# Performance work log

Measured on AMD Instinct MI355X. Metric: run time of the kernel, lower is better.

Reference implementation:

```python
import jax, jax.numpy as jnp
import numpy as np

# Qwen3MoeSparseMLPBlock config
T = 2048            # tokens
H = 2048            # hidden_size
I = 768             # moe_intermediate_size
E = 32              # num_experts
K = 8               # num_experts_per_tok
CAP = 1024          # per-expert capacity = 2 * (T*K/E); routing is ~uniform so never overflows


def setup_inputs() -> dict:
    key = jax.random.key(0)
    k1, k2, k3, k4, k5 = jax.random.split(key, 5)
    hidden_states = jax.random.normal(k1, (T, H), dtype=jnp.float32)
    gate_w = jax.random.normal(k2, (H, E), dtype=jnp.float32) / np.sqrt(H)
    gate_b = 0.01 * jax.random.normal(k3, (E,), dtype=jnp.float32)
    w_gate_up = jax.random.normal(k4, (E, H, 2 * I), dtype=jnp.float32) / np.sqrt(H)
    w_down = jax.random.normal(k5, (E, I, H), dtype=jnp.float32) / np.sqrt(I)
    return {"hidden_states": hidden_states, "gate_w": gate_w, "gate_b": gate_b,
            "w_gate_up": w_gate_up, "w_down": w_down}


def _moe(x, gate_w, gate_b, w_gate_up, w_down):
    # router: softmax in fp32, top-k, renormalize (norm_topk_prob=True)
    logits = x @ gate_w + gate_b                                   # [T, E]
    probs = jax.nn.softmax(logits.astype(jnp.float32), axis=-1)
    vals, idx = jax.lax.top_k(probs, K)                            # [T, K]
    vals = vals / jnp.sum(vals, axis=-1, keepdims=True)

    # token permutation: sort the T*K (token, expert) assignments by expert id
    A = T * K
    e_flat = idx.reshape(-1)                                       # [A] expert id per assignment
    t_flat = jnp.arange(A, dtype=jnp.int32) // K                   # [A] token id per assignment
    order = jnp.argsort(e_flat)                                    # assignments grouped by expert
    counts = jnp.bincount(e_flat, length=E)                        # [E] tokens per expert
    starts = jnp.cumsum(counts) - counts                           # [E] group offsets

    # fixed-capacity windows into the sorted assignment list (rows beyond count masked)
    win = jnp.minimum(starts[:, None] + jnp.arange(CAP)[None, :], A - 1)   # [E, CAP]
    valid = (jnp.arange(CAP)[None, :] < counts[:, None]).astype(x.dtype)   # [E, CAP]
    tok = t_flat[order][win]                                       # [E, CAP] source token ids
    w = vals.reshape(-1)[order][win] * valid                       # [E, CAP] routing weights (0 on pads)

    # gather -> grouped FFN (SiluAndMul) -> weighted scatter-add combine
    xb = x[tok]                                                    # [E, CAP, H]
    gu = jnp.einsum('ech,ehf->ecf', xb, w_gate_up)                 # [E, CAP, 2I]
    g, u = jnp.split(gu, 2, axis=-1)
    h = jax.nn.silu(g) * u                                         # [E, CAP, I]
    yb = jnp.einsum('eci,eih->ech', h, w_down) * w[..., None]      # [E, CAP, H]
    out = jnp.zeros_like(x).at[tok.reshape(-1)].add(yb.reshape(-1, H))
    return out


def reference(hidden_states, gate_w, gate_b, w_gate_up, w_down):
    return _moe(hidden_states, gate_w, gate_b, w_gate_up, w_down)
```

## Files before the change

kernel.cpp:

```cpp
#include <hip/hip_runtime.h>
#include <math.h>

#define TT 2048
#define HH 2048
#define ID 768
#define NE 32
#define KTOP 8
#define CAP 1024

typedef short bf16x8 __attribute__((ext_vector_type(8)));
typedef float f32x4 __attribute__((ext_vector_type(4)));

__device__ __forceinline__ unsigned short f2b(float f) {
  unsigned int u = __builtin_bit_cast(unsigned int, f);
  u += 0x7fff + ((u >> 16) & 1);
  return (unsigned short)(u >> 16);
}

__device__ __forceinline__ void gload16(const unsigned short* g, void* l) {
  __builtin_amdgcn_global_load_lds(
      (const __attribute__((address_space(1))) unsigned int*)g,
      (__attribute__((address_space(3))) unsigned int*)l, 16, 0, 0);
}

__global__ __launch_bounds__(256) void cvt_x_kernel(const float* __restrict__ x,
                                                    unsigned short* __restrict__ xb) {
  const size_t i = ((size_t)blockIdx.x * 256 + threadIdx.x) * 8;
  const float4 a = *(const float4*)(x + i);
  const float4 b = *(const float4*)(x + i + 4);
  union { unsigned short us[8]; uint4 v; } p;
  p.us[0] = f2b(a.x); p.us[1] = f2b(a.y); p.us[2] = f2b(a.z); p.us[3] = f2b(a.w);
  p.us[4] = f2b(b.x); p.us[5] = f2b(b.y); p.us[6] = f2b(b.z); p.us[7] = f2b(b.w);
  *(uint4*)(xb + i) = p.v;
}

__global__ __launch_bounds__(256) void cvt_w_kernel(const float* __restrict__ in,
                                                    unsigned short* __restrict__ out,
                                                    int R, int C) {
  __shared__ float tile[64][65];
  const int e = blockIdx.z;
  const int r0 = blockIdx.y * 64, c0 = blockIdx.x * 64;
  const int tid = threadIdx.x;
  const float* src = in + (size_t)e * R * C;
  const int rr = tid >> 4, c4 = tid & 15;
#pragma unroll
  for (int it = 0; it < 4; ++it) {
    const int r = it * 16 + rr;
    const float4 v = *(const float4*)(src + (size_t)(r0 + r) * C + c0 + c4 * 4);
    tile[r][c4 * 4 + 0] = v.x; tile[r][c4 * 4 + 1] = v.y;
    tile[r][c4 * 4 + 2] = v.z; tile[r][c4 * 4 + 3] = v.w;
  }
  __syncthreads();
  unsigned short* dst = out + (size_t)e * R * C;
#pragma unroll
  for (int it = 0; it < 2; ++it) {
    const int task = tid + it * 256;
    const int c = task >> 3, g = task & 7;
    union { unsigned short us[8]; uint4 v; } p;
#pragma unroll
    for (int j = 0; j < 8; ++j) p.us[j] = f2b(tile[g * 8 + j][c]);
    *(uint4*)(dst + (size_t)(c0 + c) * R + r0 + g * 8) = p.v;
  }
}

__global__ __launch_bounds__(256) void router_kernel(
    const float* __restrict__ x, const float* __restrict__ gw,
    const float* __restrict__ gb, int* __restrict__ counts,
    int* __restrict__ tok_slot, float* __restrict__ w_slot) {
  const int t = blockIdx.x;
  const int tid = threadIdx.x;
  const int e = tid & 31;
  const int c = tid >> 5;
  const float* xr = x + (size_t)t * HH;

  __shared__ double pl[8][NE];
  __shared__ float logits[NE];

  double a0 = 0.0, a1 = 0.0, a2 = 0.0, a3 = 0.0;
  const int j0 = c * 256;
#pragma unroll 4
  for (int j = 0; j < 256; j += 4) {
    const int jj = j0 + j;
    a0 = fma((double)xr[jj + 0], (double)gw[(size_t)(jj + 0) * NE + e], a0);
    a1 = fma((double)xr[jj + 1], (double)gw[(size_t)(jj + 1) * NE + e], a1);
    a2 = fma((double)xr[jj + 2], (double)gw[(size_t)(jj + 2) * NE + e], a2);
    a3 = fma((double)xr[jj + 3], (double)gw[(size_t)(jj + 3) * NE + e], a3);
  }
  pl[c][e] = (a0 + a1) + (a2 + a3);
  __syncthreads();

  if (tid < NE) {
    double s = 0.0;
    for (int cc = 0; cc < 8; ++cc) s += pl[cc][tid];
    logits[tid] = (float)s + gb[tid];
  }
  __syncthreads();

  if (tid == 0) {
    float l[NE];
    float m = -1e30f;
    for (int i = 0; i < NE; ++i) { l[i] = logits[i]; m = fmaxf(m, l[i]); }
    int sel[KTOP]; float ex[KTOP]; float s = 0.f;
    for (int k = 0; k < KTOP; ++k) {
      float best = -1e30f; int bi = 0;
      for (int i = 0; i < NE; ++i)
        if (l[i] > best) { best = l[i]; bi = i; }
      sel[k] = bi;
      ex[k] = expf(best - m);
      s += ex[k];
      l[bi] = -1e31f;
    }
    const float inv = 1.f / s;
    for (int k = 0; k < KTOP; ++k) {
      const int ee = sel[k];
      const int pos = atomicAdd(&counts[ee], 1);
      if (pos < CAP) {
        tok_slot[ee * CAP + pos] = t;
        w_slot[ee * CAP + pos] = ex[k] * inv;
      }
    }
  }
}


__global__ __launch_bounds__(256) void gu2_kernel(
    const unsigned short* __restrict__ xb, const unsigned short* __restrict__ wguT,
    const int* __restrict__ counts, const int* __restrict__ tok_slot,
    unsigned short* __restrict__ h_ws) {
  const int e = blockIdx.z, mt = blockIdx.y, nt = blockIdx.x;
  int cnt = counts[e]; cnt = cnt > CAP ? CAP : cnt;
  if (mt * 128 >= cnt) return;

  __shared__ __align__(16) unsigned short As[128 * 32];
  __shared__ __align__(16) unsigned short Bg[64 * 32];
  __shared__ __align__(16) unsigned short Bu[64 * 32];
  __shared__ int toks[128];

  const int tid = threadIdx.x;
  if (tid < 128) toks[tid] = tok_slot[e * CAP + mt * 128 + tid];
  __syncthreads();

  const unsigned short* bgp = wguT + (size_t)e * (2 * ID) * HH + (size_t)(nt * 64) * HH;
  const unsigned short* bup = bgp + (size_t)ID * HH;

  const int wv = tid >> 6;
  const int ar = tid >> 2, cg = tid & 3;
  char* ldsA0 = (char*)As + wv * 1024;
  char* ldsA1 = (char*)As + 4096 + wv * 1024;
  char* ldsBg = (char*)Bg + wv * 1024;
  char* ldsBu = (char*)Bu + wv * 1024;
  const unsigned short* srcA0 = xb + (size_t)toks[ar] * HH + cg * 8;
  const unsigned short* srcA1 = xb + (size_t)toks[ar + 64] * HH + cg * 8;
  const unsigned short* srcBg = bgp + (size_t)ar * HH + cg * 8;
  const unsigned short* srcBu = bup + (size_t)ar * HH + cg * 8;

  const int wid = tid >> 6, lane = tid & 63;
  const int wm = wid & 1, wn = wid >> 1;
  const int lr = lane & 15, quad = lane >> 4;

  f32x4 accg[4][2], accu[4][2];
  for (int s = 0; s < 4; ++s)
    for (int t = 0; t < 2; ++t)
      for (int r = 0; r < 4; ++r) { accg[s][t][r] = 0.f; accu[s][t][r] = 0.f; }

  for (int k0 = 0; k0 < HH; k0 += 32) {
    gload16(srcA0 + k0, ldsA0);
    gload16(srcA1 + k0, ldsA1);
    gload16(srcBg + k0, ldsBg);
    gload16(srcBu + k0, ldsBu);
    __syncthreads();
    bf16x8 af[4];
#pragma unroll
    for (int s = 0; s < 4; ++s)
      af[s] = *(const bf16x8*)&As[(wm * 64 + s * 16 + lr) * 32 + quad * 8];
#pragma unroll
    for (int t = 0; t < 2; ++t) {
      const bf16x8 bg = *(const bf16x8*)&Bg[(wn * 32 + t * 16 + lr) * 32 + quad * 8];
      const bf16x8 bu = *(const bf16x8*)&Bu[(wn * 32 + t * 16 + lr) * 32 + quad * 8];
#pragma unroll
      for (int s = 0; s < 4; ++s) {
        accg[s][t] = __builtin_amdgcn_mfma_f32_16x16x32_bf16(af[s], bg, accg[s][t], 0, 0, 0);
        accu[s][t] = __builtin_amdgcn_mfma_f32_16x16x32_bf16(af[s], bu, accu[s][t], 0, 0, 0);
      }
    }
    __syncthreads();
  }

  unsigned short* hb = h_ws + (size_t)(e * CAP + mt * 128) * ID + nt * 64;
#pragma unroll
  for (int s = 0; s < 4; ++s)
#pragma unroll
    for (int t = 0; t < 2; ++t)
#pragma unroll
      for (int r = 0; r < 4; ++r) {
        const int row = wm * 64 + s * 16 + quad * 4 + r;
        const int col = wn * 32 + t * 16 + lr;
        const float g = accg[s][t][r], u = accu[s][t][r];
        const float h = (g / (1.f + __expf(-g))) * u;
        hb[(size_t)row * ID + col] = f2b(h);
      }
}

__global__ __launch_bounds__(256) void down2_kernel(
    const unsigned short* __restrict__ h_ws, const unsigned short* __restrict__ wdT,
    const int* __restrict__ counts, const int* __restrict__ tok_slot,
    const float* __restrict__ w_slot, float* __restrict__ out) {
  const int e = blockIdx.z, mt = blockIdx.y;
  const int nb = blockIdx.x * 128;
  int cnt = counts[e]; cnt = cnt > CAP ? CAP : cnt;
  if (mt * 128 >= cnt) return;

  __shared__ __align__(16) unsigned short As[128 * 32];
  __shared__ __align__(16) unsigned short Bs[128 * 32];
  __shared__ int toks[128];
  __shared__ float wr[128];

  const int tid = threadIdx.x;
  if (tid < 128) {
    toks[tid] = tok_slot[e * CAP + mt * 128 + tid];
    wr[tid] = w_slot[e * CAP + mt * 128 + tid];
  }
  __syncthreads();

  const unsigned short* hb = h_ws + (size_t)(e * CAP + mt * 128) * ID;
  const unsigned short* wb = wdT + (size_t)e * HH * ID + (size_t)nb * ID;

  const int wv = tid >> 6;
  const int ar = tid >> 2, cg = tid & 3;
  char* ldsA0 = (char*)As + wv * 1024;
  char* ldsA1 = (char*)As + 4096 + wv * 1024;
  char* ldsB0 = (char*)Bs + wv * 1024;
  char* ldsB1 = (char*)Bs + 4096 + wv * 1024;
  const unsigned short* srcA0 = hb + (size_t)ar * ID + cg * 8;
  const unsigned short* srcA1 = hb + (size_t)(ar + 64) * ID + cg * 8;
  const unsigned short* srcB0 = wb + (size_t)ar * ID + cg * 8;
  const unsigned short* srcB1 = wb + (size_t)(ar + 64) * ID + cg * 8;

  const int wid = tid >> 6, lane = tid & 63;
  const int wm = wid & 1, wn = wid >> 1;
  const int lr = lane & 15, quad = lane >> 4;

  f32x4 acc[4][4];
  for (int s = 0; s < 4; ++s)
    for (int t = 0; t < 4; ++t)
      for (int r = 0; r < 4; ++r) acc[s][t][r] = 0.f;

  for (int k0 = 0; k0 < ID; k0 += 32) {
    gload16(srcA0 + k0, ldsA0);
    gload16(srcA1 + k0, ldsA1);
    gload16(srcB0 + k0, ldsB0);
    gload16(srcB1 + k0, ldsB1);
    __syncthreads();
    bf16x8 af[4], bfr[4];
#pragma unroll
    for (int s = 0; s < 4; ++s)
      af[s] = *(const bf16x8*)&As[(wm * 64 + s * 16 + lr) * 32 + quad * 8];
#pragma unroll
    for (int t = 0; t < 4; ++t)
      bfr[t] = *(const bf16x8*)&Bs[(wn * 64 + t * 16 + lr) * 32 + quad * 8];
#pragma unroll
    for (int s = 0; s < 4; ++s)
#pragma unroll
      for (int t = 0; t < 4; ++t)
        acc[s][t] = __builtin_amdgcn_mfma_f32_16x16x32_bf16(af[s], bfr[t], acc[s][t], 0, 0, 0);
    __syncthreads();
  }

#pragma unroll
  for (int s = 0; s < 4; ++s) {
#pragma unroll
    for (int r = 0; r < 4; ++r) {
      const int row = wm * 64 + s * 16 + quad * 4 + r;
      const float w = wr[row];
      if (w != 0.f) {
        const int tk = toks[row];
        float* op = out + (size_t)tk * HH + nb + wn * 64 + lr;
#pragma unroll
        for (int t = 0; t < 4; ++t)
          atomicAdd(op + t * 16, acc[s][t][r] * w);
      }
    }
  }
}


__global__ __launch_bounds__(256) void gu_kernel(
    const unsigned short* __restrict__ xb, const float* __restrict__ wgu,
    const int* __restrict__ counts, const int* __restrict__ tok_slot,
    unsigned short* __restrict__ h_ws) {
  const int e = blockIdx.z, mt = blockIdx.y, nt = blockIdx.x;
  int cnt = counts[e]; cnt = cnt > CAP ? CAP : cnt;
  if (mt * 128 >= cnt) return;

  __shared__ __align__(16) unsigned short As[128][40];
  __shared__ __align__(16) unsigned short Bg[64][40];
  __shared__ __align__(16) unsigned short Bu[64][40];
  __shared__ int toks[128];

  const int tid = threadIdx.x;
  if (tid < 128) toks[tid] = tok_slot[e * CAP + mt * 128 + tid];
  __syncthreads();

  const float* wg = wgu + (size_t)e * HH * (2 * ID) + nt * 64;
  const float* wu = wg + ID;

  const int wid = tid >> 6, lane = tid & 63;
  const int wm = wid & 1, wn = wid >> 1;
  const int lr = lane & 15, quad = lane >> 4;

  f32x4 accg[4][2], accu[4][2];
  for (int s = 0; s < 4; ++s)
    for (int t = 0; t < 2; ++t)
      for (int r = 0; r < 4; ++r) { accg[s][t][r] = 0.f; accu[s][t][r] = 0.f; }

  for (int k0 = 0; k0 < HH; k0 += 32) {
#pragma unroll
    for (int it = 0; it < 2; ++it) {
      const int task = tid + it * 256;
      const int row = task >> 2, cg = task & 3;
      const uint4 v = *(const uint4*)(xb + (size_t)toks[row] * HH + k0 + cg * 8);
      *(uint4*)&As[row][cg * 8] = v;
    }
#pragma unroll
    for (int it = 0; it < 2; ++it) {
      const int task = tid + it * 256;
      const int k = task >> 4, cg = task & 15;
      const size_t off = (size_t)(k0 + k) * (2 * ID) + cg * 4;
      const float4 vg = *(const float4*)(wg + off);
      const float4 vu = *(const float4*)(wu + off);
      Bg[cg * 4 + 0][k] = f2b(vg.x); Bg[cg * 4 + 1][k] = f2b(vg.y);
      Bg[cg * 4 + 2][k] = f2b(vg.z); Bg[cg * 4 + 3][k] = f2b(vg.w);
      Bu[cg * 4 + 0][k] = f2b(vu.x); Bu[cg * 4 + 1][k] = f2b(vu.y);
      Bu[cg * 4 + 2][k] = f2b(vu.z); Bu[cg * 4 + 3][k] = f2b(vu.w);
    }
    __syncthreads();
    bf16x8 af[4];
#pragma unroll
    for (int s = 0; s < 4; ++s)
      af[s] = *(const bf16x8*)&As[wm * 64 + s * 16 + lr][quad * 8];
#pragma unroll
    for (int t = 0; t < 2; ++t) {
      const bf16x8 bg = *(const bf16x8*)&Bg[wn * 32 + t * 16 + lr][quad * 8];
      const bf16x8 bu = *(const bf16x8*)&Bu[wn * 32 + t * 16 + lr][quad * 8];
#pragma unroll
      for (int s = 0; s < 4; ++s) {
        accg[s][t] = __builtin_amdgcn_mfma_f32_16x16x32_bf16(af[s], bg, accg[s][t], 0, 0, 0);
        accu[s][t] = __builtin_amdgcn_mfma_f32_16x16x32_bf16(af[s], bu, accu[s][t], 0, 0, 0);
      }
    }
    __syncthreads();
  }

  unsigned short* hb = h_ws + (size_t)(e * CAP + mt * 128) * ID + nt * 64;
#pragma unroll
  for (int s = 0; s < 4; ++s)
#pragma unroll
    for (int t = 0; t < 2; ++t)
#pragma unroll
      for (int r = 0; r < 4; ++r) {
        const int row = wm * 64 + s * 16 + quad * 4 + r;
        const int col = wn * 32 + t * 16 + lr;
        const float g = accg[s][t][r], u = accu[s][t][r];
        const float h = (g / (1.f + __expf(-g))) * u;
        hb[(size_t)row * ID + col] = f2b(h);
      }
}

__global__ __launch_bounds__(256) void down_kernel(
    const unsigned short* __restrict__ h_ws, const float* __restrict__ wd,
    const int* __restrict__ counts, const int* __restrict__ tok_slot,
    const float* __restrict__ w_slot, float* __restrict__ out) {
  const int e = blockIdx.z, mt = blockIdx.y;
  const int nb = blockIdx.x * 128;
  int cnt = counts[e]; cnt = cnt > CAP ? CAP : cnt;
  if (mt * 128 >= cnt) return;

  __shared__ __align__(16) unsigned short As[128][40];
  __shared__ __align__(16) unsigned short Bs[128][40];
  __shared__ int toks[128];
  __shared__ float wr[128];

  const int tid = threadIdx.x;
  if (tid < 128) {
    toks[tid] = tok_slot[e * CAP + mt * 128 + tid];
    wr[tid] = w_slot[e * CAP + mt * 128 + tid];
  }

  const unsigned short* hb = h_ws + (size_t)(e * CAP + mt * 128) * ID;
  const float* wb = wd + (size_t)e * ID * HH + nb;

  const int wid = tid >> 6, lane = tid & 63;
  const int wm = wid & 1, wn = wid >> 1;
  const int lr = lane & 15, quad = lane >> 4;

  f32x4 acc[4][4];
  for (int s = 0; s < 4; ++s)
    for (int t = 0; t < 4; ++t)
      for (int r = 0; r < 4; ++r) acc[s][t][r] = 0.f;

  for (int k0 = 0; k0 < ID; k0 += 32) {
#pragma unroll
    for (int it = 0; it < 2; ++it) {
      const int task = tid + it * 256;
      const int row = task >> 2, cg = task & 3;
      const uint4 v = *(const uint4*)(hb + (size_t)row * ID + k0 + cg * 8);
      *(uint4*)&As[row][cg * 8] = v;
    }
#pragma unroll
    for (int it = 0; it < 4; ++it) {
      const int task = tid + it * 256;
      const int k = task >> 5, cg = task & 31;
      const float4 v = *(const float4*)(wb + (size_t)(k0 + k) * HH + cg * 4);
      Bs[cg * 4 + 0][k] = f2b(v.x); Bs[cg * 4 + 1][k] = f2b(v.y);
      Bs[cg * 4 + 2][k] = f2b(v.z); Bs[cg * 4 + 3][k] = f2b(v.w);
    }
    __syncthreads();
    bf16x8 af[4], bfr[4];
#pragma unroll
    for (int s = 0; s < 4; ++s)
      af[s] = *(const bf16x8*)&As[wm * 64 + s * 16 + lr][quad * 8];
#pragma unroll
    for (int t = 0; t < 4; ++t)
      bfr[t] = *(const bf16x8*)&Bs[wn * 64 + t * 16 + lr][quad * 8];
#pragma unroll
    for (int s = 0; s < 4; ++s)
#pragma unroll
      for (int t = 0; t < 4; ++t)
        acc[s][t] = __builtin_amdgcn_mfma_f32_16x16x32_bf16(af[s], bfr[t], acc[s][t], 0, 0, 0);
    __syncthreads();
  }

#pragma unroll
  for (int s = 0; s < 4; ++s) {
#pragma unroll
    for (int r = 0; r < 4; ++r) {
      const int row = wm * 64 + s * 16 + quad * 4 + r;
      const float w = wr[row];
      if (w != 0.f) {
        const int tk = toks[row];
        float* op = out + (size_t)tk * HH + nb + wn * 64 + lr;
#pragma unroll
        for (int t = 0; t < 4; ++t)
          atomicAdd(op + t * 16, acc[s][t][r] * w);
      }
    }
  }
}

extern "C" void kernel_launch(void* const* d_in, const int* in_sizes, int n_in,
                              void* d_out, int out_size, void* d_ws, size_t ws_size,
                              hipStream_t stream) {
  const float* x   = (const float*)d_in[0];
  const float* gw  = (const float*)d_in[1];
  const float* gb  = (const float*)d_in[2];
  const float* wgu = (const float*)d_in[3];
  const float* wd  = (const float*)d_in[4];
  float* out = (float*)d_out;

  char* ws = (char*)d_ws;
  int*   counts   = (int*)ws;
  int*   tok_slot = (int*)(ws + 256);
  float* w_slot   = (float*)(ws + 256 + 131072);
  unsigned short* xb   = (unsigned short*)(ws + 262656);
  unsigned short* h_ws = (unsigned short*)(ws + 8651264);
  unsigned short* wguT = (unsigned short*)(ws + 58982912);
  unsigned short* wdT  = (unsigned short*)(ws + 260309504);
  const size_t NEED = 360972800ULL;

  hipMemsetAsync(d_ws, 0, 262400, stream);
  hipMemsetAsync(d_out, 0, (size_t)out_size * sizeof(float), stream);

  cvt_x_kernel<<<dim3((TT * HH) / (256 * 8)), dim3(256), 0, stream>>>(x, xb);
  router_kernel<<<dim3(TT), dim3(256), 0, stream>>>(x, gw, gb, counts, tok_slot, w_slot);

  if (ws_size >= NEED) {
    cvt_w_kernel<<<dim3((2 * ID) / 64, HH / 64, NE), dim3(256), 0, stream>>>(wgu, wguT, HH, 2 * ID);
    cvt_w_kernel<<<dim3(HH / 64, ID / 64, NE), dim3(256), 0, stream>>>(wd, wdT, ID, HH);
    gu2_kernel<<<dim3(ID / 64, CAP / 128, NE), dim3(256), 0, stream>>>(xb, wguT, counts, tok_slot, h_ws);
    down2_kernel<<<dim3(HH / 128, CAP / 128, NE), dim3(256), 0, stream>>>(h_ws, wdT, counts, tok_slot, w_slot, out);
  } else {
    gu_kernel<<<dim3(ID / 64, CAP / 128, NE), dim3(256), 0, stream>>>(xb, wgu, counts, tok_slot, h_ws);
    down_kernel<<<dim3(HH / 128, CAP / 128, NE), dim3(256), 0, stream>>>(h_ws, wd, counts, tok_slot, w_slot, out);
  }
}
```

Baseline: 1.147 ms.

## Replace grouped GEMMs with 256x256 double-buffered, swizzled, 8-wave MFMA kernels

Rewrites the gate-up and down grouped GEMM kernels to use 512-thread blocks computing 256x256 output tiles with 64-wide K steps. Global-to-LDS loads are double-buffered and interleaved with MFMA quadrants under manual barriers and vmcnt waits, and the LDS layout uses an XOR swizzle to avoid bank conflicts. The gate-up weights are reordered during conversion so gate and up columns sit in interleaved 128-column blocks, letting one tile produce both halves for SiLU fusion. The bigger tiles add data reuse and hide load latency, at the cost of high LDS and register pressure and wasted work on partially filled 256-row tiles.

```diff
diff --git a/kernel.cpp b/kernel.cpp
--- a/kernel.cpp
+++ b/kernel.cpp
@@ -22,6 +22,9 @@
       (const __attribute__((address_space(1))) unsigned int*)g,
       (__attribute__((address_space(3))) unsigned int*)l, 16, 0, 0);
 }
+
+#define SBAR() asm volatile("s_barrier" ::: "memory")
+#define VMCNT(n) asm volatile("s_waitcnt vmcnt(" #n ")" ::: "memory")
 
 __global__ __launch_bounds__(256) void cvt_x_kernel(const float* __restrict__ x,
                                                     unsigned short* __restrict__ xb) {
@@ -60,6 +63,37 @@
 #pragma unroll
     for (int j = 0; j < 8; ++j) p.us[j] = f2b(tile[g * 8 + j][c]);
     *(uint4*)(dst + (size_t)(c0 + c) * R + r0 + g * 8) = p.v;
+  }
+}
+
+__global__ __launch_bounds__(256) void cvt_wgu_kernel(const float* __restrict__ in,
+                                                      unsigned short* __restrict__ out) {
+  __shared__ float tile[64][65];
+  const int e = blockIdx.z;
+  const int r0 = blockIdx.y * 64, c0 = blockIdx.x * 64;
+  const int tid = threadIdx.x;
+  const float* src = in + (size_t)e * HH * (2 * ID);
+  const int rr = tid >> 4, c4 = tid & 15;
+#pragma unroll
+  for (int it = 0; it < 4; ++it) {
+    const int r = it * 16 + rr;
+    const float4 v = *(const float4*)(src + (size_t)(r0 + r) * (2 * ID) + c0 + c4 * 4);
+    tile[r][c4 * 4 + 0] = v.x; tile[r][c4 * 4 + 1] = v.y;
+    tile[r][c4 * 4 + 2] = v.z; tile[r][c4 * 4 + 3] = v.w;
+  }
+  __syncthreads();
+  unsigned short* dst = out + (size_t)e * HH * (2 * ID);
+#pragma unroll
+  for (int it = 0; it < 2; ++it) {
+    const int task = tid + it * 256;
+    const int c = task >> 3, g = task & 7;
+    const int n = c0 + c;
+    const int dr = (n < ID) ? ((n >> 7) * 256 + (n & 127))
+                            : (((n - ID) >> 7) * 256 + 128 + ((n - ID) & 127));
+    union { unsigned short us[8]; uint4 v; } p;
+#pragma unroll
+    for (int j = 0; j < 8; ++j) p.us[j] = f2b(tile[g * 8 + j][c]);
+    *(uint4*)(dst + (size_t)dr * HH + r0 + g * 8) = p.v;
   }
 }
 
@@ -123,164 +157,262 @@
 }
 
 
-__global__ __launch_bounds__(256) void gu2_kernel(
+#define STG_A(nb, half, k0)                                                   \
+  do {                                                                        \
+    gload16(A_src[(half) * 2 + 0] + (k0), &Asb[nb][half][w * 512]);           \
+    gload16(A_src[(half) * 2 + 1] + (k0), &Asb[nb][half][4096 + w * 512]);    \
+  } while (0)
+#define STG_B(nb, half, k0)                                                   \
+  do {                                                                        \
+    gload16(B_src[(half) * 2 + 0] + (k0), &Bsb[nb][half][w * 512]);           \
+    gload16(B_src[(half) * 2 + 1] + (k0), &Bsb[nb][half][4096 + w * 512]);    \
+  } while (0)
+
+#define MFMA16(QM, QN)                                                        \
+  do {                                                                        \
+    _Pragma("unroll")                                                         \
+    for (int m = 0; m < 4; ++m) {                                             \
+      _Pragma("unroll")                                                       \
+      for (int n = 0; n < 2; ++n) {                                           \
+        acc[QM][QN][m][n] = __builtin_amdgcn_mfma_f32_16x16x32_bf16(          \
+            af[m][0], bf[n][0], acc[QM][QN][m][n], 0, 0, 0);                  \
+        acc[QM][QN][m][n] = __builtin_amdgcn_mfma_f32_16x16x32_bf16(          \
+            af[m][1], bf[n][1], acc[QM][QN][m][n], 0, 0, 0);                  \
+      }                                                                       \
+    }                                                                         \
+  } while (0)
+
+#define LDA(half)                                                             \
+  do {                                                                        \
+    _Pragma("unroll")                                                         \
+    for (int m = 0; m < 4; ++m) {                                             \
+      af[m][0] = *(const bf16x8*)&Asb[buf][half][(arow + m * 16) * 64 + cs0f];\
+      af[m][1] = *(const bf16x8*)&Asb[buf][half][(arow + m * 16) * 64 + cs1f];\
+    }                                                                         \
+  } while (0)
+#define LDB(half)                                                             \
+  do {                                                                        \
+    _Pragma("unroll")                                                         \
+    for (int n = 0; n < 2; ++n) {                                             \
+      bf[n][0] = *(const bf16x8*)&Bsb[buf][half][(brow + n * 16) * 64 + cs0f];\
+      bf[n][1] = *(const bf16x8*)&Bsb[buf][half][(brow + n * 16) * 64 + cs1f];\
+    }                                                                         \
+  } while (0)
+
+__global__ __launch_bounds__(512, 2) void gu3_kernel(
     const unsigned short* __restrict__ xb, const unsigned short* __restrict__ wguT,
     const int* __restrict__ counts, const int* __restrict__ tok_slot,
     unsigned short* __restrict__ h_ws) {
   const int e = blockIdx.z, mt = blockIdx.y, nt = blockIdx.x;
   int cnt = counts[e]; cnt = cnt > CAP ? CAP : cnt;
-  if (mt * 128 >= cnt) return;
-
-  __shared__ __align__(16) unsigned short As[128 * 32];
-  __shared__ __align__(16) unsigned short Bg[64 * 32];
-  __shared__ __align__(16) unsigned short Bu[64 * 32];
-  __shared__ int toks[128];
+  if (mt * 256 >= cnt) return;
+
+  __shared__ __align__(16) unsigned short Asb[2][2][128 * 64];
+  __shared__ __align__(16) unsigned short Bsb[2][2][128 * 64];
 
   const int tid = threadIdx.x;
-  if (tid < 128) toks[tid] = tok_slot[e * CAP + mt * 128 + tid];
-  __syncthreads();
-
-  const unsigned short* bgp = wguT + (size_t)e * (2 * ID) * HH + (size_t)(nt * 64) * HH;
-  const unsigned short* bup = bgp + (size_t)ID * HH;
-
-  const int wv = tid >> 6;
-  const int ar = tid >> 2, cg = tid & 3;
-  char* ldsA0 = (char*)As + wv * 1024;
-  char* ldsA1 = (char*)As + 4096 + wv * 1024;
-  char* ldsBg = (char*)Bg + wv * 1024;
-  char* ldsBu = (char*)Bu + wv * 1024;
-  const unsigned short* srcA0 = xb + (size_t)toks[ar] * HH + cg * 8;
-  const unsigned short* srcA1 = xb + (size_t)toks[ar + 64] * HH + cg * 8;
-  const unsigned short* srcBg = bgp + (size_t)ar * HH + cg * 8;
-  const unsigned short* srcBu = bup + (size_t)ar * HH + cg * 8;
-
-  const int wid = tid >> 6, lane = tid & 63;
-  const int wm = wid & 1, wn = wid >> 1;
+  const int w = tid >> 6, lane = tid & 63;
+  const int wr = w & 1, wc = w >> 1;
   const int lr = lane & 15, quad = lane >> 4;
 
-  f32x4 accg[4][2], accu[4][2];
-  for (int s = 0; s < 4; ++s)
-    for (int t = 0; t < 2; ++t)
-      for (int r = 0; r < 4; ++r) { accg[s][t][r] = 0.f; accu[s][t][r] = 0.f; }
-
-  for (int k0 = 0; k0 < HH; k0 += 32) {
-    gload16(srcA0 + k0, ldsA0);
-    gload16(srcA1 + k0, ldsA1);
-    gload16(srcBg + k0, ldsBg);
-    gload16(srcBu + k0, ldsBu);
-    __syncthreads();
-    bf16x8 af[4];
-#pragma unroll
-    for (int s = 0; s < 4; ++s)
-      af[s] = *(const bf16x8*)&As[(wm * 64 + s * 16 + lr) * 32 + quad * 8];
-#pragma unroll
-    for (int t = 0; t < 2; ++t) {
-      const bf16x8 bg = *(const bf16x8*)&Bg[(wn * 32 + t * 16 + lr) * 32 + quad * 8];
-      const bf16x8 bu = *(const bf16x8*)&Bu[(wn * 32 + t * 16 + lr) * 32 + quad * 8];
-#pragma unroll
-      for (int s = 0; s < 4; ++s) {
-        accg[s][t] = __builtin_amdgcn_mfma_f32_16x16x32_bf16(af[s], bg, accg[s][t], 0, 0, 0);
-        accu[s][t] = __builtin_amdgcn_mfma_f32_16x16x32_bf16(af[s], bu, accu[s][t], 0, 0, 0);
+  const int ra = tid >> 3, ca = tid & 7;
+  const int cs = (ca ^ (ra & 7)) * 8;
+
+  const int* tsl = tok_slot + e * CAP + mt * 256;
+  const unsigned short* A_src[4];
+  A_src[0] = xb + (size_t)tsl[ra] * HH + cs;
+  A_src[1] = xb + (size_t)tsl[64 + ra] * HH + cs;
+  A_src[2] = xb + (size_t)tsl[128 + ra] * HH + cs;
+  A_src[3] = xb + (size_t)tsl[192 + ra] * HH + cs;
+  const unsigned short* bb = wguT + (size_t)e * (2 * ID) * HH + (size_t)(nt * 256) * HH;
+  const unsigned short* B_src[4];
+  B_src[0] = bb + (size_t)ra * HH + cs;
+  B_src[1] = bb + (size_t)(64 + ra) * HH + cs;
+  B_src[2] = bb + (size_t)(128 + ra) * HH + cs;
+  B_src[3] = bb + (size_t)(192 + ra) * HH + cs;
+
+  const int cs0f = (quad ^ (lr & 7)) * 8;
+  const int cs1f = ((4 + quad) ^ (lr & 7)) * 8;
+  const int arow = wr * 64 + lr;
+  const int brow = wc * 32 + lr;
+
+  f32x4 acc[2][2][4][2];
+#pragma unroll
+  for (int a = 0; a < 2; ++a)
+#pragma unroll
+    for (int b = 0; b < 2; ++b)
+#pragma unroll
+      for (int m = 0; m < 4; ++m)
+#pragma unroll
+        for (int n = 0; n < 2; ++n)
+#pragma unroll
+          for (int r = 0; r < 4; ++r) acc[a][b][m][n][r] = 0.f;
+
+  STG_A(0, 0, 0); STG_B(0, 0, 0); STG_A(0, 1, 0); STG_B(0, 1, 0);
+  VMCNT(0);
+  SBAR();
+
+  bf16x8 af[4][2], bf[2][2];
+  for (int t = 0; t < 32; ++t) {
+    const int buf = t & 1, nb = buf ^ 1;
+    const int kn = (t + 1) * 64;
+    const bool pf = (t + 1) < 32;
+    LDA(0); LDB(0);
+    if (pf) { STG_A(nb, 0, kn); STG_B(nb, 0, kn); }
+    SBAR();
+    __builtin_amdgcn_s_setprio(1);
+    MFMA16(0, 0);
+    __builtin_amdgcn_s_setprio(0);
+    VMCNT(4);
+    SBAR();
+    LDB(1);
+    if (pf) { STG_A(nb, 1, kn); STG_B(nb, 1, kn); }
+    SBAR();
+    __builtin_amdgcn_s_setprio(1);
+    MFMA16(0, 1);
+    __builtin_amdgcn_s_setprio(0);
+    SBAR();
+    LDA(1); LDB(0);
+    SBAR();
+    __builtin_amdgcn_s_setprio(1);
+    MFMA16(1, 0);
+    __builtin_amdgcn_s_setprio(0);
+    SBAR();
+    LDB(1);
+    SBAR();
+    __builtin_amdgcn_s_setprio(1);
+    MFMA16(1, 1);
+    __builtin_amdgcn_s_setprio(0);
+    VMCNT(2);
+    SBAR();
+  }
+
+  unsigned short* hb = h_ws + ((size_t)e * CAP + mt * 256) * ID + nt * 128;
+#pragma unroll
+  for (int qm = 0; qm < 2; ++qm)
+#pragma unroll
+    for (int m = 0; m < 4; ++m)
+#pragma unroll
+      for (int r = 0; r < 4; ++r) {
+        const int row = qm * 128 + wr * 64 + m * 16 + quad * 4 + r;
+#pragma unroll
+        for (int n = 0; n < 2; ++n) {
+          const float g = acc[qm][0][m][n][r], u = acc[qm][1][m][n][r];
+          const float h = (g / (1.f + __expf(-g))) * u;
+          hb[(size_t)row * ID + wc * 32 + n * 16 + lr] = f2b(h);
+        }
       }
-    }
-    __syncthreads();
-  }
-
-  unsigned short* hb = h_ws + (size_t)(e * CAP + mt * 128) * ID + nt * 64;
-#pragma unroll
-  for (int s = 0; s < 4; ++s)
-#pragma unroll
-    for (int t = 0; t < 2; ++t)
-#pragma unroll
-      for (int r = 0; r < 4; ++r) {
-        const int row = wm * 64 + s * 16 + quad * 4 + r;
-        const int col = wn * 32 + t * 16 + lr;
-        const float g = accg[s][t][r], u = accu[s][t][r];
-        const float h = (g / (1.f + __expf(-g))) * u;
-        hb[(size_t)row * ID + col] = f2b(h);
-      }
-}
-
-__global__ __launch_bounds__(256) void down2_kernel(
+}
+
+__global__ __launch_bounds__(512, 2) void down3_kernel(
     const unsigned short* __restrict__ h_ws, const unsigned short* __restrict__ wdT,
     const int* __restrict__ counts, const int* __restrict__ tok_slot,
     const float* __restrict__ w_slot, float* __restrict__ out) {
-  const int e = blockIdx.z, mt = blockIdx.y;
-  const int nb = blockIdx.x * 128;
+  const int e = blockIdx.z, mt = blockIdx.y, nt = blockIdx.x;
   int cnt = counts[e]; cnt = cnt > CAP ? CAP : cnt;
-  if (mt * 128 >= cnt) return;
-
-  __shared__ __align__(16) unsigned short As[128 * 32];
-  __shared__ __align__(16) unsigned short Bs[128 * 32];
-  __shared__ int toks[128];
-  __shared__ float wr[128];
+  if (mt * 256 >= cnt) return;
+
+  __shared__ __align__(16) unsigned short Asb[2][2][128 * 64];
+  __shared__ __align__(16) unsigned short Bsb[2][2][128 * 64];
 
   const int tid = threadIdx.x;
-  if (tid < 128) {
-    toks[tid] = tok_slot[e * CAP + mt * 128 + tid];
-    wr[tid] = w_slot[e * CAP + mt * 128 + tid];
-  }
-  __syncthreads();
-
-  const unsigned short* hb = h_ws + (size_t)(e * CAP + mt * 128) * ID;
-  const unsigned short* wb = wdT + (size_t)e * HH * ID + (size_t)nb * ID;
-
-  const int wv = tid >> 6;
-  const int ar = tid >> 2, cg = tid & 3;
-  char* ldsA0 = (char*)As + wv * 1024;
-  char* ldsA1 = (char*)As + 4096 + wv * 1024;
-  char* ldsB0 = (char*)Bs + wv * 1024;
-  char* ldsB1 = (char*)Bs + 4096 + wv * 1024;
-  const unsigned short* srcA0 = hb + (size_t)ar * ID + cg * 8;
-  const unsigned short* srcA1 = hb + (size_t)(ar + 64) * ID + cg * 8;
-  const unsigned short* srcB0 = wb + (size_t)ar * ID + cg * 8;
-  const unsigned short* srcB1 = wb + (size_t)(ar + 64) * ID + cg * 8;
-
-  const int wid = tid >> 6, lane = tid & 63;
-  const int wm = wid & 1, wn = wid >> 1;
+  const int w = tid >> 6, lane = tid & 63;
+  const int wr = w & 1, wc = w >> 1;
   const int lr = lane & 15, quad = lane >> 4;
 
-  f32x4 acc[4][4];
-  for (int s = 0; s < 4; ++s)
-    for (int t = 0; t < 4; ++t)
-      for (int r = 0; r < 4; ++r) acc[s][t][r] = 0.f;
-
-  for (int k0 = 0; k0 < ID; k0 += 32) {
-    gload16(srcA0 + k0, ldsA0);
-    gload16(srcA1 + k0, ldsA1);
-    gload16(srcB0 + k0, ldsB0);
-    gload16(srcB1 + k0, ldsB1);
-    __syncthreads();
-    bf16x8 af[4], bfr[4];
-#pragma unroll
-    for (int s = 0; s < 4; ++s)
-      af[s] = *(const bf16x8*)&As[(wm * 64 + s * 16 + lr) * 32 + quad * 8];
-#pragma unroll
-    for (int t = 0; t < 4; ++t)
-      bfr[t] = *(const bf16x8*)&Bs[(wn * 64 + t * 16 + lr) * 32 + quad * 8];
-#pragma unroll
-    for (int s = 0; s < 4; ++s)
-#pragma unroll
-      for (int t = 0; t < 4; ++t)
-        acc[s][t] = __builtin_amdgcn_mfma_f32_16x16x32_bf16(af[s], bfr[t], acc[s][t], 0, 0, 0);
-    __syncthreads();
-  }
-
-#pragma unroll
-  for (int s = 0; s < 4; ++s) {
-#pragma unroll
-    for (int r = 0; r < 4; ++r) {
-      const int row = wm * 64 + s * 16 + quad * 4 + r;
-      const float w = wr[row];
-      if (w != 0.f) {
-        const int tk = toks[row];
-        float* op = out + (size_t)tk * HH + nb + wn * 64 + lr;
-#pragma unroll
-        for (int t = 0; t < 4; ++t)
-          atomicAdd(op + t * 16, acc[s][t][r] * w);
+  const int ra = tid >> 3, ca = tid & 7;
+  const int cs = (ca ^ (ra & 7)) * 8;
+
+  const unsigned short* hb = h_ws + ((size_t)e * CAP + mt * 256) * ID;
+  const unsigned short* A_src[4];
+  A_src[0] = hb + (size_t)ra * ID + cs;
+  A_src[1] = hb + (size_t)(64 + ra) * ID + cs;
+  A_src[2] = hb + (size_t)(128 + ra) * ID + cs;
+  A_src[3] = hb + (size_t)(192 + ra) * ID + cs;
+  const unsigned short* wb = wdT + (size_t)e * HH * ID + (size_t)(nt * 256) * ID;
+  const unsigned short* B_src[4];
+  B_src[0] = wb + (size_t)ra * ID + cs;
+  B_src[1] = wb + (size_t)(64 + ra) * ID + cs;
+  B_src[2] = wb + (size_t)(128 + ra) * ID + cs;
+  B_src[3] = wb + (size_t)(192 + ra) * ID + cs;
+
+  const int cs0f = (quad ^ (lr & 7)) * 8;
+  const int cs1f = ((4 + quad) ^ (lr & 7)) * 8;
+  const int arow = wr * 64 + lr;
+  const int brow = wc * 32 + lr;
+
+  f32x4 acc[2][2][4][2];
+#pragma unroll
+  for (int a = 0; a < 2; ++a)
+#pragma unroll
+    for (int b = 0; b < 2; ++b)
+#pragma unroll
+      for (int m = 0; m < 4; ++m)
+#pragma unroll
+        for (int n = 0; n < 2; ++n)
+#pragma unroll
+          for (int r = 0; r < 4; ++r) acc[a][b][m][n][r] = 0.f;
+
+  STG_A(0, 0, 0); STG_B(0, 0, 0); STG_A(0, 1, 0); STG_B(0, 1, 0);
+  VMCNT(0);
+  SBAR();
+
+  bf16x8 af[4][2], bf[2][2];
+  for (int t = 0; t < 12; ++t) {
+    const int buf = t & 1, nb = buf ^ 1;
+    const int kn = (t + 1) * 64;
+    const bool pf = (t + 1) < 12;
+    LDA(0); LDB(0);
+    if (pf) { STG_A(nb, 0, kn); STG_B(nb, 0, kn); }
+    SBAR();
+    __builtin_amdgcn_s_setprio(1);
+    MFMA16(0, 0);
+    __builtin_amdgcn_s_setprio(0);
+    VMCNT(4);
+    SBAR();
+    LDB(1);
+    if (pf) { STG_A(nb, 1, kn); STG_B(nb, 1, kn); }
+    SBAR();
+    __builtin_amdgcn_s_setprio(1);
+    MFMA16(0, 1);
+    __builtin_amdgcn_s_setprio(0);
+    SBAR();
+    LDA(1); LDB(0);
+    SBAR();
+    __builtin_amdgcn_s_setprio(1);
+    MFMA16(1, 0);
+    __builtin_amdgcn_s_setprio(0);
+    SBAR();
+    LDB(1);
+    SBAR();
+    __builtin_amdgcn_s_setprio(1);
+    MFMA16(1, 1);
+    __builtin_amdgcn_s_setprio(0);
+    VMCNT(2);
+    SBAR();
+  }
+
+  const int* tsl = tok_slot + e * CAP + mt * 256;
+  const float* wsl = w_slot + e * CAP + mt * 256;
+#pragma unroll
+  for (int qm = 0; qm < 2; ++qm)
+#pragma unroll
+    for (int m = 0; m < 4; ++m)
+#pragma unroll
+      for (int r = 0; r < 4; ++r) {
+        const int row = qm * 128 + wr * 64 + m * 16 + quad * 4 + r;
+        const float wgt = wsl[row];
+        if (wgt != 0.f) {
+          const int tk = tsl[row];
+          float* op = out + (size_t)tk * HH + nt * 256;
+#pragma unroll
+          for (int qn = 0; qn < 2; ++qn)
+#pragma unroll
+            for (int n = 0; n < 2; ++n)
+              atomicAdd(op + qn * 128 + wc * 32 + n * 16 + lr,
+                        acc[qm][qn][m][n][r] * wgt);
+        }
       }
-    }
-  }
 }
 
 
@@ -474,10 +606,12 @@
   router_kernel<<<dim3(TT), dim3(256), 0, stream>>>(x, gw, gb, counts, tok_slot, w_slot);
 
   if (ws_size >= NEED) {
-    cvt_w_kernel<<<dim3((2 * ID) / 64, HH / 64, NE), dim3(256), 0, stream>>>(wgu, wguT, HH, 2 * ID);
+    cvt_wgu_kernel<<<dim3((2 * ID) / 64, HH / 64, NE), dim3(256), 0, stream>>>(wgu, wguT);
     cvt_w_kernel<<<dim3(HH / 64, ID / 64, NE), dim3(256), 0, stream>>>(wd, wdT, ID, HH);
-    gu2_kernel<<<dim3(ID / 64, CAP / 128, NE), dim3(256), 0, stream>>>(xb, wguT, counts, tok_slot, h_ws);
-    down2_kernel<<<dim3(HH / 128, CAP / 128, NE), dim3(256), 0, stream>>>(h_ws, wdT, counts, tok_slot, w_slot, out);
+    gu3_kernel<<<dim3((2 * ID) / 256, CAP / 256, NE), dim3(512), 0, stream>>>(
+        xb, wguT, counts, tok_slot, h_ws);
+    down3_kernel<<<dim3(HH / 256, CAP / 256, NE), dim3(512), 0, stream>>>(
+        h_ws, wdT, counts, tok_slot, w_slot, out);
   } else {
     gu_kernel<<<dim3(ID / 64, CAP / 128, NE), dim3(256), 0, stream>>>(xb, wgu, counts, tok_slot, h_ws);
     down_kernel<<<dim3(HH / 128, CAP / 128, NE), dim3(256), 0, stream>>>(h_ws, wd, counts, tok_slot, w_slot, out);
```

New measurement: 1.267 ms. 1.1x slower.

## Widen K tiles with swizzled LDS and replace atomic scatter with combine pass

Applied to the files above, without the earlier changes.

The gate-up and down GEMM kernels now stage 64-wide K slices per iteration instead of 32. LDS column offsets are XOR-swizzled to cut bank conflicts and halve the barrier count per K step. The down kernel no longer issues float atomicAdds into the output. It writes weighted rows into a per-slot fp32 buffer, the router records each token's slot indices, and a new combine kernel sums the eight slots per token. This also drops the output memset on the fast path, but it needs a much larger workspace: if that size is not provided, execution falls back to the old slow kernels.

```diff
diff --git a/kernel.cpp b/kernel.cpp
--- a/kernel.cpp
+++ b/kernel.cpp
@@ -66,7 +66,8 @@
 __global__ __launch_bounds__(256) void router_kernel(
     const float* __restrict__ x, const float* __restrict__ gw,
     const float* __restrict__ gb, int* __restrict__ counts,
-    int* __restrict__ tok_slot, float* __restrict__ w_slot) {
+    int* __restrict__ tok_slot, float* __restrict__ w_slot,
+    int* __restrict__ inv) {
   const int t = blockIdx.x;
   const int tid = threadIdx.x;
   const int e = tid & 31;
@@ -110,20 +111,23 @@
       s += ex[k];
       l[bi] = -1e31f;
     }
-    const float inv = 1.f / s;
+    const float inv_s = 1.f / s;
     for (int k = 0; k < KTOP; ++k) {
       const int ee = sel[k];
       const int pos = atomicAdd(&counts[ee], 1);
       if (pos < CAP) {
         tok_slot[ee * CAP + pos] = t;
-        w_slot[ee * CAP + pos] = ex[k] * inv;
-      }
-    }
-  }
-}
-
-
-__global__ __launch_bounds__(256) void gu2_kernel(
+        w_slot[ee * CAP + pos] = ex[k] * inv_s;
+        inv[t * KTOP + k] = ee * CAP + pos;
+      } else {
+        inv[t * KTOP + k] = -1;
+      }
+    }
+  }
+}
+
+
+__global__ __launch_bounds__(256) void gu4_kernel(
     const unsigned short* __restrict__ xb, const unsigned short* __restrict__ wguT,
     const int* __restrict__ counts, const int* __restrict__ tok_slot,
     unsigned short* __restrict__ h_ws) {
@@ -131,57 +135,77 @@
   int cnt = counts[e]; cnt = cnt > CAP ? CAP : cnt;
   if (mt * 128 >= cnt) return;
 
-  __shared__ __align__(16) unsigned short As[128 * 32];
-  __shared__ __align__(16) unsigned short Bg[64 * 32];
-  __shared__ __align__(16) unsigned short Bu[64 * 32];
+  __shared__ __align__(16) unsigned short As[128 * 64];
+  __shared__ __align__(16) unsigned short Bg[64 * 64];
+  __shared__ __align__(16) unsigned short Bu[64 * 64];
   __shared__ int toks[128];
 
   const int tid = threadIdx.x;
   if (tid < 128) toks[tid] = tok_slot[e * CAP + mt * 128 + tid];
   __syncthreads();
 
+  const int w = tid >> 6, lane = tid & 63;
+  const int wm = w & 1, wn = w >> 1;
+  const int lr = lane & 15, quad = lane >> 4;
+
+  const int ra = tid >> 3;
+  const int sw = ((tid & 7) ^ (ra & 7)) * 8;
+
+  const unsigned short* srcA[4];
+#pragma unroll
+  for (int i = 0; i < 4; ++i)
+    srcA[i] = xb + (size_t)toks[i * 32 + ra] * HH + sw;
   const unsigned short* bgp = wguT + (size_t)e * (2 * ID) * HH + (size_t)(nt * 64) * HH;
   const unsigned short* bup = bgp + (size_t)ID * HH;
-
-  const int wv = tid >> 6;
-  const int ar = tid >> 2, cg = tid & 3;
-  char* ldsA0 = (char*)As + wv * 1024;
-  char* ldsA1 = (char*)As + 4096 + wv * 1024;
-  char* ldsBg = (char*)Bg + wv * 1024;
-  char* ldsBu = (char*)Bu + wv * 1024;
-  const unsigned short* srcA0 = xb + (size_t)toks[ar] * HH + cg * 8;
-  const unsigned short* srcA1 = xb + (size_t)toks[ar + 64] * HH + cg * 8;
-  const unsigned short* srcBg = bgp + (size_t)ar * HH + cg * 8;
-  const unsigned short* srcBu = bup + (size_t)ar * HH + cg * 8;
-
-  const int wid = tid >> 6, lane = tid & 63;
-  const int wm = wid & 1, wn = wid >> 1;
-  const int lr = lane & 15, quad = lane >> 4;
+  const unsigned short* srcBg[2];
+  const unsigned short* srcBu[2];
+#pragma unroll
+  for (int i = 0; i < 2; ++i) {
+    srcBg[i] = bgp + (size_t)(i * 32 + ra) * HH + sw;
+    srcBu[i] = bup + (size_t)(i * 32 + ra) * HH + sw;
+  }
+
+  const int cs0f = ((quad) ^ (lr & 7)) * 8;
+  const int cs1f = ((4 + quad) ^ (lr & 7)) * 8;
 
   f32x4 accg[4][2], accu[4][2];
+#pragma unroll
   for (int s = 0; s < 4; ++s)
+#pragma unroll
     for (int t = 0; t < 2; ++t)
+#pragma unroll
       for (int r = 0; r < 4; ++r) { accg[s][t][r] = 0.f; accu[s][t][r] = 0.f; }
 
-  for (int k0 = 0; k0 < HH; k0 += 32) {
-    gload16(srcA0 + k0, ldsA0);
-    gload16(srcA1 + k0, ldsA1);
-    gload16(srcBg + k0, ldsBg);
-    gload16(srcBu + k0, ldsBu);
-    __syncthreads();
-    bf16x8 af[4];
-#pragma unroll
-    for (int s = 0; s < 4; ++s)
-      af[s] = *(const bf16x8*)&As[(wm * 64 + s * 16 + lr) * 32 + quad * 8];
-#pragma unroll
-    for (int t = 0; t < 2; ++t) {
-      const bf16x8 bg = *(const bf16x8*)&Bg[(wn * 32 + t * 16 + lr) * 32 + quad * 8];
-      const bf16x8 bu = *(const bf16x8*)&Bu[(wn * 32 + t * 16 + lr) * 32 + quad * 8];
-#pragma unroll
-      for (int s = 0; s < 4; ++s) {
-        accg[s][t] = __builtin_amdgcn_mfma_f32_16x16x32_bf16(af[s], bg, accg[s][t], 0, 0, 0);
-        accu[s][t] = __builtin_amdgcn_mfma_f32_16x16x32_bf16(af[s], bu, accu[s][t], 0, 0, 0);
-      }
+  for (int k0 = 0; k0 < HH; k0 += 64) {
+#pragma unroll
+    for (int i = 0; i < 4; ++i)
+      gload16(srcA[i] + k0, (char*)As + i * 4096 + w * 1024);
+#pragma unroll
+    for (int i = 0; i < 2; ++i)
+      gload16(srcBg[i] + k0, (char*)Bg + i * 4096 + w * 1024);
+#pragma unroll
+    for (int i = 0; i < 2; ++i)
+      gload16(srcBu[i] + k0, (char*)Bu + i * 4096 + w * 1024);
+    __syncthreads();
+#pragma unroll
+    for (int sl = 0; sl < 2; ++sl) {
+      const int cf = sl ? cs1f : cs0f;
+      bf16x8 af[4], bg[2], bu[2];
+#pragma unroll
+      for (int s = 0; s < 4; ++s)
+        af[s] = *(const bf16x8*)&As[(wm * 64 + s * 16 + lr) * 64 + cf];
+#pragma unroll
+      for (int t = 0; t < 2; ++t) {
+        bg[t] = *(const bf16x8*)&Bg[(wn * 32 + t * 16 + lr) * 64 + cf];
+        bu[t] = *(const bf16x8*)&Bu[(wn * 32 + t * 16 + lr) * 64 + cf];
+      }
+#pragma unroll
+      for (int t = 0; t < 2; ++t)
+#pragma unroll
+        for (int s = 0; s < 4; ++s) {
+          accg[s][t] = __builtin_amdgcn_mfma_f32_16x16x32_bf16(af[s], bg[t], accg[s][t], 0, 0, 0);
+          accu[s][t] = __builtin_amdgcn_mfma_f32_16x16x32_bf16(af[s], bu[t], accu[s][t], 0, 0, 0);
+        }
     }
     __syncthreads();
   }
@@ -201,86 +225,116 @@
       }
 }
 
-__global__ __launch_bounds__(256) void down2_kernel(
+__global__ __launch_bounds__(256) void down4_kernel(
     const unsigned short* __restrict__ h_ws, const unsigned short* __restrict__ wdT,
-    const int* __restrict__ counts, const int* __restrict__ tok_slot,
-    const float* __restrict__ w_slot, float* __restrict__ out) {
+    const int* __restrict__ counts, const float* __restrict__ w_slot,
+    float* __restrict__ y_ws) {
   const int e = blockIdx.z, mt = blockIdx.y;
   const int nb = blockIdx.x * 128;
   int cnt = counts[e]; cnt = cnt > CAP ? CAP : cnt;
   if (mt * 128 >= cnt) return;
 
-  __shared__ __align__(16) unsigned short As[128 * 32];
-  __shared__ __align__(16) unsigned short Bs[128 * 32];
-  __shared__ int toks[128];
+  __shared__ __align__(16) unsigned short As[128 * 64];
+  __shared__ __align__(16) unsigned short Bs[128 * 64];
   __shared__ float wr[128];
 
   const int tid = threadIdx.x;
-  if (tid < 128) {
-    toks[tid] = tok_slot[e * CAP + mt * 128 + tid];
-    wr[tid] = w_slot[e * CAP + mt * 128 + tid];
-  }
-  __syncthreads();
+  if (tid < 128) wr[tid] = w_slot[e * CAP + mt * 128 + tid];
+
+  const int w = tid >> 6, lane = tid & 63;
+  const int wm = w & 1, wn = w >> 1;
+  const int lr = lane & 15, quad = lane >> 4;
+
+  const int ra = tid >> 3;
+  const int sw = ((tid & 7) ^ (ra & 7)) * 8;
 
   const unsigned short* hb = h_ws + (size_t)(e * CAP + mt * 128) * ID;
   const unsigned short* wb = wdT + (size_t)e * HH * ID + (size_t)nb * ID;
-
-  const int wv = tid >> 6;
-  const int ar = tid >> 2, cg = tid & 3;
-  char* ldsA0 = (char*)As + wv * 1024;
-  char* ldsA1 = (char*)As + 4096 + wv * 1024;
-  char* ldsB0 = (char*)Bs + wv * 1024;
-  char* ldsB1 = (char*)Bs + 4096 + wv * 1024;
-  const unsigned short* srcA0 = hb + (size_t)ar * ID + cg * 8;
-  const unsigned short* srcA1 = hb + (size_t)(ar + 64) * ID + cg * 8;
-  const unsigned short* srcB0 = wb + (size_t)ar * ID + cg * 8;
-  const unsigned short* srcB1 = wb + (size_t)(ar + 64) * ID + cg * 8;
-
-  const int wid = tid >> 6, lane = tid & 63;
-  const int wm = wid & 1, wn = wid >> 1;
-  const int lr = lane & 15, quad = lane >> 4;
+  const unsigned short* srcA[4];
+  const unsigned short* srcB[4];
+#pragma unroll
+  for (int i = 0; i < 4; ++i) {
+    srcA[i] = hb + (size_t)(i * 32 + ra) * ID + sw;
+    srcB[i] = wb + (size_t)(i * 32 + ra) * ID + sw;
+  }
+
+  const int cs0f = ((quad) ^ (lr & 7)) * 8;
+  const int cs1f = ((4 + quad) ^ (lr & 7)) * 8;
 
   f32x4 acc[4][4];
+#pragma unroll
   for (int s = 0; s < 4; ++s)
+#pragma unroll
     for (int t = 0; t < 4; ++t)
+#pragma unroll
       for (int r = 0; r < 4; ++r) acc[s][t][r] = 0.f;
 
-  for (int k0 = 0; k0 < ID; k0 += 32) {
-    gload16(srcA0 + k0, ldsA0);
-    gload16(srcA1 + k0, ldsA1);
-    gload16(srcB0 + k0, ldsB0);
-    gload16(srcB1 + k0, ldsB1);
-    __syncthreads();
-    bf16x8 af[4], bfr[4];
-#pragma unroll
-    for (int s = 0; s < 4; ++s)
-      af[s] = *(const bf16x8*)&As[(wm * 64 + s * 16 + lr) * 32 + quad * 8];
-#pragma unroll
-    for (int t = 0; t < 4; ++t)
-      bfr[t] = *(const bf16x8*)&Bs[(wn * 64 + t * 16 + lr) * 32 + quad * 8];
-#pragma unroll
-    for (int s = 0; s < 4; ++s)
+  for (int k0 = 0; k0 < ID; k0 += 64) {
+#pragma unroll
+    for (int i = 0; i < 4; ++i)
+      gload16(srcA[i] + k0, (char*)As + i * 4096 + w * 1024);
+#pragma unroll
+    for (int i = 0; i < 4; ++i)
+      gload16(srcB[i] + k0, (char*)Bs + i * 4096 + w * 1024);
+    __syncthreads();
+#pragma unroll
+    for (int sl = 0; sl < 2; ++sl) {
+      const int cf = sl ? cs1f : cs0f;
+      bf16x8 af[4], bfr[4];
+#pragma unroll
+      for (int s = 0; s < 4; ++s)
+        af[s] = *(const bf16x8*)&As[(wm * 64 + s * 16 + lr) * 64 + cf];
 #pragma unroll
       for (int t = 0; t < 4; ++t)
-        acc[s][t] = __builtin_amdgcn_mfma_f32_16x16x32_bf16(af[s], bfr[t], acc[s][t], 0, 0, 0);
-    __syncthreads();
-  }
-
+        bfr[t] = *(const bf16x8*)&Bs[(wn * 64 + t * 16 + lr) * 64 + cf];
+#pragma unroll
+      for (int s = 0; s < 4; ++s)
+#pragma unroll
+        for (int t = 0; t < 4; ++t)
+          acc[s][t] = __builtin_amdgcn_mfma_f32_16x16x32_bf16(af[s], bfr[t], acc[s][t], 0, 0, 0);
+    }
+    __syncthreads();
+  }
+
+  const size_t slot0 = (size_t)e * CAP + mt * 128;
 #pragma unroll
   for (int s = 0; s < 4; ++s) {
 #pragma unroll
     for (int r = 0; r < 4; ++r) {
       const int row = wm * 64 + s * 16 + quad * 4 + r;
-      const float w = wr[row];
-      if (w != 0.f) {
-        const int tk = toks[row];
-        float* op = out + (size_t)tk * HH + nb + wn * 64 + lr;
+      const float wgt = wr[row];
+      if (wgt != 0.f) {
+        float* op = y_ws + (slot0 + row) * HH + nb + wn * 64 + lr;
 #pragma unroll
         for (int t = 0; t < 4; ++t)
-          atomicAdd(op + t * 16, acc[s][t][r] * w);
-      }
-    }
-  }
+          op[t * 16] = acc[s][t][r] * wgt;
+      }
+    }
+  }
+}
+
+__global__ __launch_bounds__(256) void combine_kernel(
+    const float* __restrict__ y_ws, const int* __restrict__ inv,
+    float* __restrict__ out) {
+  const int t = blockIdx.x;
+  const int c = threadIdx.x;
+  int sl[KTOP];
+#pragma unroll
+  for (int k = 0; k < KTOP; ++k) sl[k] = inv[t * KTOP + k];
+  float4 s0 = {0.f, 0.f, 0.f, 0.f}, s1 = {0.f, 0.f, 0.f, 0.f};
+#pragma unroll
+  for (int k = 0; k < KTOP; ++k) {
+    if (sl[k] >= 0) {
+      const float* yr = y_ws + (size_t)sl[k] * HH + c * 8;
+      const float4 a = *(const float4*)yr;
+      const float4 b = *(const float4*)(yr + 4);
+      s0.x += a.x; s0.y += a.y; s0.z += a.z; s0.w += a.w;
+      s1.x += b.x; s1.y += b.y; s1.z += b.z; s1.w += b.w;
+    }
+  }
+  float* op = out + (size_t)t * HH + c * 8;
+  *(float4*)op = s0;
+  *(float4*)(op + 4) = s1;
 }
 
 
@@ -460,25 +514,28 @@
   char* ws = (char*)d_ws;
   int*   counts   = (int*)ws;
   int*   tok_slot = (int*)(ws + 256);
-  float* w_slot   = (float*)(ws + 256 + 131072);
-  unsigned short* xb   = (unsigned short*)(ws + 262656);
-  unsigned short* h_ws = (unsigned short*)(ws + 8651264);
-  unsigned short* wguT = (unsigned short*)(ws + 58982912);
-  unsigned short* wdT  = (unsigned short*)(ws + 260309504);
-  const size_t NEED = 360972800ULL;
-
-  hipMemsetAsync(d_ws, 0, 262400, stream);
-  hipMemsetAsync(d_out, 0, (size_t)out_size * sizeof(float), stream);
+  float* w_slot   = (float*)(ws + 131328);
+  int*   inv      = (int*)(ws + 262400);
+  unsigned short* xb   = (unsigned short*)(ws + 327936);
+  unsigned short* h_ws = (unsigned short*)(ws + 8716544);
+  unsigned short* wguT = (unsigned short*)(ws + 59048192);
+  unsigned short* wdT  = (unsigned short*)(ws + 260374784);
+  float*          y_ws = (float*)(ws + 361038080);
+  const size_t NEED = 629473536ULL;
+
+  hipMemsetAsync(d_ws, 0, 327936, stream);
 
   cvt_x_kernel<<<dim3((TT * HH) / (256 * 8)), dim3(256), 0, stream>>>(x, xb);
-  router_kernel<<<dim3(TT), dim3(256), 0, stream>>>(x, gw, gb, counts, tok_slot, w_slot);
+  router_kernel<<<dim3(TT), dim3(256), 0, stream>>>(x, gw, gb, counts, tok_slot, w_slot, inv);
 
   if (ws_size >= NEED) {
     cvt_w_kernel<<<dim3((2 * ID) / 64, HH / 64, NE), dim3(256), 0, stream>>>(wgu, wguT, HH, 2 * ID);
     cvt_w_kernel<<<dim3(HH / 64, ID / 64, NE), dim3(256), 0, stream>>>(wd, wdT, ID, HH);
-    gu2_kernel<<<dim3(ID / 64, CAP / 128, NE), dim3(256), 0, stream>>>(xb, wguT, counts, tok_slot, h_ws);
-    down2_kernel<<<dim3(HH / 128, CAP / 128, NE), dim3(256), 0, stream>>>(h_ws, wdT, counts, tok_slot, w_slot, out);
+    gu4_kernel<<<dim3(ID / 64, CAP / 128, NE), dim3(256), 0, stream>>>(xb, wguT, counts, tok_slot, h_ws);
+    down4_kernel<<<dim3(HH / 128, CAP / 128, NE), dim3(256), 0, stream>>>(h_ws, wdT, counts, w_slot, y_ws);
+    combine_kernel<<<dim3(TT), dim3(256), 0, stream>>>(y_ws, inv, out);
   } else {
+    hipMemsetAsync(d_out, 0, (size_t)out_size * sizeof(float), stream);
     gu_kernel<<<dim3(ID / 64, CAP / 128, NE), dim3(256), 0, stream>>>(xb, wgu, counts, tok_slot, h_ws);
     down_kernel<<<dim3(HH / 128, CAP / 128, NE), dim3(256), 0, stream>>>(h_ws, wd, counts, tok_slot, w_slot, out);
   }
```

Result: faster. 1.122 ms (-2.2%).
